# Kernel optimization log

Measured on AMD Instinct MI355X. Metric: run time of the kernel, lower is better.

The kernel has to match this reference:

```python
import jax, jax.numpy as jnp
import numpy as np

N_TOKENS = 50257  # vocab size (init kwarg)


def setup_inputs() -> dict:
    key = jax.random.key(0)
    # [batch, seq] int token ids in [0, N_TOKENS)
    inputs = jax.random.randint(key, (1024, 512), 0, N_TOKENS, dtype=jnp.int32)
    return {"inputs": inputs}


def reference(inputs) -> jnp.ndarray:
    # Faithful math: sum_j one_hot(inputs[b, j], N_TOKENS) -> token count histogram,
    # then drop token id 0 (padding). Implemented as a scatter-add instead of
    # materializing the [B, S, V] one-hot tensor.
    B, S = inputs.shape
    rows = jnp.arange(B, dtype=jnp.int32)[:, None]  # [B, 1] broadcast against [B, S]
    counts = jnp.zeros((B, N_TOKENS), dtype=jnp.float32)
    counts = counts.at[rows, inputs].add(jnp.float32(1.0))  # [B, V]
    return counts[:, 1:]  # drop token id 0, matches [:, 1:] in the original
```

## Files before the change

kernel.cpp:

```cpp
#include <hip/hip_runtime.h>


#define BATCH 1024
#define SEQ 512
#define VOCAB 50257
#define OUT_COLS (VOCAB - 1)
#define OUT_FLOATS ((size_t)BATCH * OUT_COLS)
#define OUT_F4 (OUT_FLOATS / 4)

#define ZERO_BLOCKS 2048
#define BLOCK 256

__global__ __launch_bounds__(BLOCK) void bow_zero_kernel(float4* __restrict__ out) {
    size_t i = (size_t)blockIdx.x * BLOCK + threadIdx.x;
    const size_t stride = (size_t)ZERO_BLOCKS * BLOCK;
    const float4 z = make_float4(0.0f, 0.0f, 0.0f, 0.0f);
    for (; i < OUT_F4; i += stride) {
        out[i] = z;
    }
}

__global__ __launch_bounds__(BLOCK) void bow_scatter_kernel(
    const int* __restrict__ tokens, float* __restrict__ out) {
    const int gid = blockIdx.x * BLOCK + threadIdx.x;
    const int tok = tokens[gid];
    if (tok != 0) {
        const int b = gid >> 9;
        atomicAdd(out + (size_t)b * OUT_COLS + (tok - 1), 1.0f);
    }
}

extern "C" void kernel_launch(void* const* d_in, const int* in_sizes, int n_in,
                              void* d_out, int out_size, void* d_ws, size_t ws_size,
                              hipStream_t stream) {
    const int* tokens = (const int*)d_in[0];
    float* out = (float*)d_out;

    bow_zero_kernel<<<dim3(ZERO_BLOCKS), dim3(BLOCK), 0, stream>>>((float4*)out);
    bow_scatter_kernel<<<dim3((BATCH * SEQ) / BLOCK), dim3(BLOCK), 0, stream>>>(
        tokens, out);
}
```

Before: 225.3 us.

## Replace global atomic scatter with per-row LDS histogram in vocab chunks

Result: faster. 206.1 us (-8.5%).

```diff
diff --git a/kernel.cpp b/kernel.cpp
--- a/kernel.cpp
+++ b/kernel.cpp
@@ -7,9 +7,17 @@
 #define OUT_COLS (VOCAB - 1)
 #define OUT_FLOATS ((size_t)BATCH * OUT_COLS)
 #define OUT_F4 (OUT_FLOATS / 4)
+#define CHUNK 4096
+#define NCHUNK 13
+#define BLOCK 256
+#define ZERO_BLOCKS 2048
 
-#define ZERO_BLOCKS 2048
-#define BLOCK 256
+#define LDS_BAR()                                              \
+    do {                                                       \
+        asm volatile("s_waitcnt lgkmcnt(0)" ::: "memory");     \
+        __builtin_amdgcn_s_barrier();                          \
+        asm volatile("" ::: "memory");                         \
+    } while (0)
 
 __global__ __launch_bounds__(BLOCK) void bow_zero_kernel(float4* __restrict__ out) {
     size_t i = (size_t)blockIdx.x * BLOCK + threadIdx.x;
@@ -20,13 +28,49 @@
     }
 }
 
-__global__ __launch_bounds__(BLOCK) void bow_scatter_kernel(
+__global__ __launch_bounds__(BLOCK) void bow_sparse_kernel(
     const int* __restrict__ tokens, float* __restrict__ out) {
-    const int gid = blockIdx.x * BLOCK + threadIdx.x;
-    const int tok = tokens[gid];
-    if (tok != 0) {
-        const int b = gid >> 9;
-        atomicAdd(out + (size_t)b * OUT_COLS + (tok - 1), 1.0f);
+    __shared__ unsigned int hist[CHUNK];
+
+    const int t = threadIdx.x;
+    const int b = blockIdx.x;
+
+    const uint4 z4 = make_uint4(0u, 0u, 0u, 0u);
+    #pragma unroll
+    for (int k = 0; k < 4; ++k)
+        *(uint4*)&hist[t * 4 + k * (BLOCK * 4)] = z4;
+
+    const int2 tk = ((const int2*)(tokens + (size_t)b * SEQ))[t];
+    const unsigned int cx = (unsigned int)(tk.x - 1);
+    const unsigned int cy = (unsigned int)(tk.y - 1);
+
+    float* orow = out + (size_t)b * OUT_COLS;
+
+    LDS_BAR();
+
+    for (int c = 0; c < NCHUNK; ++c) {
+        const unsigned int c0 = (unsigned int)c * CHUNK;
+
+        const unsigned int rx = cx - c0;
+        const unsigned int ry = cy - c0;
+        bool wx = false, wy = false;
+        if (rx < CHUNK) wx = (atomicAdd(&hist[rx], 1u) == 0u);
+        if (ry < CHUNK) wy = (atomicAdd(&hist[ry], 1u) == 0u);
+
+        LDS_BAR();
+
+        if (wx) {
+            const unsigned int cnt = hist[rx];
+            orow[c0 + rx] = (float)cnt;
+            hist[rx] = 0u;
+        }
+        if (wy) {
+            const unsigned int cnt = hist[ry];
+            orow[c0 + ry] = (float)cnt;
+            hist[ry] = 0u;
+        }
+
+        LDS_BAR();
     }
 }
 
@@ -37,6 +81,5 @@
     float* out = (float*)d_out;
 
     bow_zero_kernel<<<dim3(ZERO_BLOCKS), dim3(BLOCK), 0, stream>>>((float4*)out);
-    bow_scatter_kernel<<<dim3((BATCH * SEQ) / BLOCK), dim3(BLOCK), 0, stream>>>(
-        tokens, out);
+    bow_sparse_kernel<<<dim3(BATCH), dim3(BLOCK), 0, stream>>>(tokens, out);
 }
```
